# Kernel tuning notes

Measured on AMD Instinct MI355X. Metric: run time of the kernel, lower is better.

The kernel has to match this reference:

```python
import jax, jax.numpy as jnp
import numpy as np
import math

N = 20000          # nodes (residues)
E = 640000         # edges
CS = 384           # c_s
CZ = 128           # c_z
CH = 16            # c_hidden
H = 8              # no_heads
PQK = 8            # no_qk_points == no_v_points (forced equal, see notes)
FS = 128           # scalar channels in feat_irreps
PIN = 16           # vector channels in feat_irreps
HC = H * CH        # 128
HPQ = H * PQK * 3  # 192
CZ4 = CZ // 4      # 32
OUT_IN = HC + 3 * H + H + H * CZ4  # 416 actual concat width
INF = 100000.0
EPS = 1e-8


def setup_inputs() -> dict:
    key = jax.random.key(0)
    ks = jax.random.split(key, 16)
    w = lambda k, i, o: (jax.random.normal(k, (i, o), jnp.float32) / np.float32(np.sqrt(i)))
    frame_s = jax.random.normal(ks[0], (N, CS), jnp.float32)
    tfn_t = jax.random.normal(ks[1], (N, FS + 3 * PIN), jnp.float32)
    z = jax.random.normal(ks[2], (E, CZ), jnp.float32)
    edge_index = jax.random.randint(ks[3], (2, E), 0, N)
    mask = jnp.ones((N,), jnp.float32)
    # Rigid transforms: proper-ish rotations via QR, translations
    rot, _ = jnp.linalg.qr(jax.random.normal(ks[4], (N, 3, 3), jnp.float32))
    trans = jax.random.normal(ks[5], (N, 3), jnp.float32)
    return {
        "frame_s": frame_s, "tfn_t": tfn_t, "z": z,
        "edge_index": edge_index, "mask": mask,
        "rot": rot, "trans": trans,
        "Wq": w(ks[6], CS, HC), "bq": jnp.zeros((HC,), jnp.float32),
        "Wk_s": w(ks[7], FS, HC), "Wk_v": w(ks[8], PIN, PQK),
        "Wqp": w(ks[9], CS, HPQ), "bqp": jnp.zeros((HPQ,), jnp.float32),
        "Wb": w(ks[10], CZ, H), "bb": jnp.zeros((H,), jnp.float32),
        "Wdz": w(ks[11], CZ, CZ4), "bdz": jnp.zeros((CZ4,), jnp.float32),
        # ipa_point_weights_init_: softplus(hw) == 1  =>  hw = log(e - 1)
        "head_weights": jnp.full((H,), np.float32(np.log(np.e - 1.0))),
        "Wout": w(ks[12], OUT_IN, CS), "bout": jnp.zeros((CS,), jnp.float32),
    }


def _segment_softmax(a, seg, n):
    # pyg-style numerically stable segment softmax over edges grouped by seg
    m = jax.ops.segment_max(a, seg, num_segments=n)
    m = jnp.where(jnp.isfinite(m), m, 0.0)
    e = jnp.exp(a - m[seg])
    s = jax.ops.segment_sum(e, seg, num_segments=n)
    return e / (s[seg] + 1e-16)


def _forward(frame_s, tfn_t, z, mask, rot, trans,
             Wq, bq, Wk_s, Wk_v, Wqp, bqp, Wb, bb, Wdz, bdz,
             head_weights, Wout, bout, edge_index):
    n = frame_s.shape[0]
    src = edge_index[1]
    dst = edge_index[0]

    # scalar queries: [N,H,C]
    q = (frame_s @ Wq + bq).reshape(n, H, CH)

    # o3.Linear (feat_irreps -> k_irreps): scalars mix scalars, vectors mix vectors.
    # NOTE: original code uses linear_k for BOTH k and v (faithful bug), so v==k.
    scal = tfn_t[:, :FS]
    vecs = tfn_t[:, FS:].reshape(n, PIN, 3)
    k_scal = scal @ Wk_s                                   # [N, HC]
    k_vec = jnp.einsum('npx,pq->nqx', vecs, Wk_v)          # [N, PQK, 3]
    k = k_scal.reshape(n, H, CH)
    v = k
    k_tail = k_vec.reshape(n, PQK * 3)                     # [N, 24]
    # torch: split([3]*PQK) then stack(dim=-1) -> [N,3,PQK], then view [N,H,-1,3]
    k_pts = jnp.stack(jnp.split(k_tail, PQK, axis=-1), axis=-1)  # [N,3,PQK]
    k_pts = k_pts.reshape(n, H, -1, 3)                     # [N,H,1,3]
    v_pts = k_pts

    # query points, rigid-transformed: [N,H,PQK,3]
    q_pts = frame_s @ Wqp + bqp                            # [N, 3*H*PQK]
    q_pts = jnp.stack(jnp.split(q_pts, 3, axis=-1), axis=-1)  # [N, H*PQK, 3]
    q_pts = jnp.einsum('nij,npj->npi', rot, q_pts) + trans[:, None, :]
    q_pts = q_pts.reshape(n, H, PQK, 3)

    # scalar attention logits [E,H]
    a = jnp.einsum('ehc,ehc->eh', q[src], k[dst])
    a = a * np.float32(math.sqrt(1.0 / (3 * CH)))
    b = z @ Wb + bb                                        # [E,H]
    a = a + np.float32(math.sqrt(1.0 / 3)) * b

    # point attention: disp [E,H,PQK,3] (k_pts broadcasts over points)
    disp = q_pts[src] - k_pts[dst]
    pt_att = jnp.sum(disp * disp, axis=-1)                 # [E,H,PQK]
    hw = jax.nn.softplus(head_weights) * np.float32(math.sqrt(1.0 / (3 * (PQK * 9.0 / 2))))
    pt_att = -0.5 * jnp.sum(pt_att * hw[None, :, None], axis=-1)  # [E,H]

    edge_mask = INF * (mask[dst] * mask[src] - 1.0)        # [E]
    a = a + pt_att + edge_mask[:, None]

    a = _segment_softmax(a, src, n)                        # [E,H]

    # scalar output
    o = jax.ops.segment_sum(a[..., None] * v[dst], src, num_segments=n)  # [N,H,C]
    o = o.reshape(n, HC)

    # point output
    o_pt = jax.ops.segment_sum(a[:, :, None, None] * v_pts[dst], src, num_segments=n)  # [N,H,1,3]
    o_pt = jnp.einsum('nji,nhpj->nhpi', rot, o_pt - trans[:, None, None, :])  # invert_apply
    o_pt_norm = jnp.sqrt(jnp.sum(o_pt * o_pt, axis=-1) + EPS).reshape(n, H)
    o_pt = o_pt.reshape(n, -1, 3)                          # [N,H,3]

    # pair output
    pair_z = z @ Wdz + bdz                                 # [E,CZ4]
    o_pair = jax.ops.segment_sum(a[..., None] * pair_z[:, None, :], src, num_segments=n)  # [N,H,CZ4]
    o_pair = o_pair.reshape(n, H * CZ4)

    feats = jnp.concatenate(
        [o, o_pt[..., 0], o_pt[..., 1], o_pt[..., 2], o_pt_norm, o_pair], axis=-1)  # [N,416]
    return feats @ Wout + bout                             # [N, CS]


def reference(frame_s, tfn_t, z, edge_index, mask, rot, trans,
              Wq, bq, Wk_s, Wk_v, Wqp, bqp, Wb, bb, Wdz, bdz,
              head_weights, Wout, bout):
    return _forward(frame_s, tfn_t, z, mask, rot, trans,
                    Wq, bq, Wk_s, Wk_v, Wqp, bqp, Wb, bb, Wdz, bdz,
                    head_weights, Wout, bout, edge_index)
```

## Files before the change

kernel.cpp:

```cpp
#include <hip/hip_runtime.h>
#include <math.h>

typedef __attribute__((ext_vector_type(8))) short short8;
typedef __attribute__((ext_vector_type(4))) float f32x4;

static __device__ inline unsigned short f2bf(float f) {
    union { float f; unsigned u; } v; v.f = f;
    unsigned r = v.u + 0x7FFF + ((v.u >> 16) & 1);
    return (unsigned short)(r >> 16);
}

template<int WJ>
__device__ __forceinline__ void gemm_body(
    unsigned short* __restrict__ As, unsigned short* __restrict__ Bs,
    const float* __restrict__ A, int lda,
    const float* __restrict__ BT, int ldb,
    const float* __restrict__ bias,
    float* __restrict__ C, int ldc,
    int M, int N, int K, int bx, int by)
{
    constexpr int GBN = WJ * 32;
    const int t = threadIdx.x;
    const int wid = t >> 6, lane = t & 63;
    const int wm = (wid & 1) * 64;
    const int wn = (wid >> 1) * (WJ * 16);
    const int row16 = lane & 15, quad = lane >> 4;
    const int bm = bx * 128;
    const int bn = by * GBN;

    f32x4 acc[4][WJ];
    #pragma unroll
    for (int i = 0; i < 4; ++i)
        #pragma unroll
        for (int j = 0; j < WJ; ++j)
            #pragma unroll
            for (int r = 0; r < 4; ++r) acc[i][j][r] = 0.f;

    const int ktiles = (K + 63) >> 6;
    for (int kt = 0; kt < ktiles; ++kt) {
        const int k0 = kt << 6;
        #pragma unroll
        for (int it = 0; it < 8; ++it) {
            int f = it * 256 + t;
            int row = f >> 4, kq = (f & 15) << 2;
            float4 av = make_float4(0.f, 0.f, 0.f, 0.f);
            if (bm + row < M && k0 + kq < K)
                av = *(const float4*)(A + (size_t)(bm + row) * lda + k0 + kq);
            ushort4 uv;
            uv.x = f2bf(av.x); uv.y = f2bf(av.y); uv.z = f2bf(av.z); uv.w = f2bf(av.w);
            *(ushort4*)(&As[row * 72 + kq]) = uv;
        }
        #pragma unroll
        for (int it = 0; it < WJ * 2; ++it) {
            int f = it * 256 + t;
            int row = f >> 4, kq = (f & 15) << 2;
            float4 bv = make_float4(0.f, 0.f, 0.f, 0.f);
            if (bn + row < N && k0 + kq < K)
                bv = *(const float4*)(BT + (size_t)(bn + row) * ldb + k0 + kq);
            ushort4 uv;
            uv.x = f2bf(bv.x); uv.y = f2bf(bv.y); uv.z = f2bf(bv.z); uv.w = f2bf(bv.w);
            *(ushort4*)(&Bs[row * 72 + kq]) = uv;
        }
        __syncthreads();

        #pragma unroll
        for (int ks = 0; ks < 64; ks += 32) {
            short8 af[4], bfv[WJ];
            #pragma unroll
            for (int i = 0; i < 4; ++i)
                af[i] = *(const short8*)(&As[(wm + i * 16 + row16) * 72 + ks + quad * 8]);
            #pragma unroll
            for (int j = 0; j < WJ; ++j)
                bfv[j] = *(const short8*)(&Bs[(wn + j * 16 + row16) * 72 + ks + quad * 8]);
            #pragma unroll
            for (int i = 0; i < 4; ++i)
                #pragma unroll
                for (int j = 0; j < WJ; ++j)
                    acc[i][j] = __builtin_amdgcn_mfma_f32_16x16x32_bf16(af[i], bfv[j], acc[i][j], 0, 0, 0);
        }
        __syncthreads();
    }

    #pragma unroll
    for (int i = 0; i < 4; ++i)
        #pragma unroll
        for (int j = 0; j < WJ; ++j) {
            int col = bn + wn + j * 16 + row16;
            if (col >= N) continue;
            float bv = bias ? bias[col] : 0.f;
            #pragma unroll
            for (int r = 0; r < 4; ++r) {
                int row = bm + wm + i * 16 + quad * 4 + r;
                if (row < M) C[(size_t)row * ldc + col] = acc[i][j][r] + bv;
            }
        }
}

template<int WJ>
__global__ __launch_bounds__(256) void gemm_mfma(
    const float* __restrict__ A, int lda,
    const float* __restrict__ BT, int ldb,
    const float* __restrict__ bias,
    float* __restrict__ C, int ldc,
    int M, int N, int K)
{
    __shared__ unsigned short As[128 * 72];
    __shared__ unsigned short Bs[WJ * 32 * 72];
    gemm_body<WJ>(As, Bs, A, lda, BT, ldb, bias, C, ldc, M, N, K, blockIdx.x, blockIdx.y);
}

__global__ __launch_bounds__(256) void bpair_stream(
    const float* __restrict__ z, const float* __restrict__ wcatT,
    const float* __restrict__ bcat, float* __restrict__ bpair, int E)
{
    const int lane = threadIdx.x & 63;
    const int wid = threadIdx.x >> 6;
    const int row16 = lane & 15, quad = lane >> 4;

    short8 bfv[3][4];
    float bj[3];
    #pragma unroll
    for (int j = 0; j < 3; ++j) {
        int col = j * 16 + row16;
        bool cv = col < 40;
        bj[j] = cv ? bcat[col] : 0.f;
        #pragma unroll
        for (int ks = 0; ks < 4; ++ks) {
            float4 w0 = make_float4(0.f, 0.f, 0.f, 0.f);
            float4 w1 = make_float4(0.f, 0.f, 0.f, 0.f);
            if (cv) {
                const float* wp = wcatT + (size_t)col * 128 + ks * 32 + quad * 8;
                w0 = *(const float4*)(wp);
                w1 = *(const float4*)(wp + 4);
            }
            short8 f;
            f[0] = (short)f2bf(w0.x); f[1] = (short)f2bf(w0.y);
            f[2] = (short)f2bf(w0.z); f[3] = (short)f2bf(w0.w);
            f[4] = (short)f2bf(w1.x); f[5] = (short)f2bf(w1.y);
            f[6] = (short)f2bf(w1.z); f[7] = (short)f2bf(w1.w);
            bfv[j][ks] = f;
        }
    }

    const int nstrips = (E + 31) >> 5;
    const int gw = blockIdx.x * 4 + wid;
    const int nw = gridDim.x * 4;
    for (int st = gw; st < nstrips; st += nw) {
        const int r0 = st * 32;
        short8 af[2][4];
        #pragma unroll
        for (int i = 0; i < 2; ++i) {
            int row = r0 + i * 16 + row16;
            bool rv = row < E;
            const float* zp = z + (size_t)row * 128 + quad * 8;
            #pragma unroll
            for (int ks = 0; ks < 4; ++ks) {
                float4 a0 = make_float4(0.f, 0.f, 0.f, 0.f);
                float4 a1 = make_float4(0.f, 0.f, 0.f, 0.f);
                if (rv) {
                    a0 = *(const float4*)(zp + ks * 32);
                    a1 = *(const float4*)(zp + ks * 32 + 4);
                }
                short8 f;
                f[0] = (short)f2bf(a0.x); f[1] = (short)f2bf(a0.y);
                f[2] = (short)f2bf(a0.z); f[3] = (short)f2bf(a0.w);
                f[4] = (short)f2bf(a1.x); f[5] = (short)f2bf(a1.y);
                f[6] = (short)f2bf(a1.z); f[7] = (short)f2bf(a1.w);
                af[i][ks] = f;
            }
        }

        f32x4 acc[2][3];
        #pragma unroll
        for (int i = 0; i < 2; ++i)
            #pragma unroll
            for (int j = 0; j < 3; ++j)
                #pragma unroll
                for (int r = 0; r < 4; ++r) acc[i][j][r] = 0.f;

        #pragma unroll
        for (int ks = 0; ks < 4; ++ks)
            #pragma unroll
            for (int i = 0; i < 2; ++i)
                #pragma unroll
                for (int j = 0; j < 3; ++j)
                    acc[i][j] = __builtin_amdgcn_mfma_f32_16x16x32_bf16(af[i][ks], bfv[j][ks], acc[i][j], 0, 0, 0);

        #pragma unroll
        for (int i = 0; i < 2; ++i)
            #pragma unroll
            for (int j = 0; j < 3; ++j) {
                int col = j * 16 + row16;
                if (col >= 40) continue;
                #pragma unroll
                for (int r = 0; r < 4; ++r) {
                    int row = r0 + i * 16 + quad * 4 + r;
                    if (row < E) bpair[(size_t)row * 40 + col] = acc[i][j][r] + bj[j];
                }
            }
    }
}

__global__ __launch_bounds__(256) void mega_kernel(
    const float* __restrict__ frame_s, const float* __restrict__ wqqpT,
    const float* __restrict__ bqqp, float* __restrict__ qqp, int n,
    const float* __restrict__ tfn, const float* __restrict__ wksT,
    float* __restrict__ kbuf,
    const float* __restrict__ Wkv, float* __restrict__ kpts,
    const int* __restrict__ srcA, int* __restrict__ cur, int* __restrict__ elist, int E,
    int nb_qqp_x, int nb_qqp, int nb_k, int nb_kpts)
{
    __shared__ unsigned short As[128 * 72];
    __shared__ unsigned short Bs[128 * 72];
    int b = blockIdx.x;
    if (b < nb_qqp) {
        gemm_body<4>(As, Bs, frame_s, 384, wqqpT, 384, bqqp, qqp, 320, n, 320, 384,
                     b % nb_qqp_x, b / nb_qqp_x);
        return;
    }
    b -= nb_qqp;
    if (b < nb_k) {
        gemm_body<4>(As, Bs, tfn, 176, wksT, 128, nullptr, kbuf, 128, n, 128, 128, b, 0);
        return;
    }
    b -= nb_k;
    if (b < nb_kpts) {
        int t = b * 256 + threadIdx.x;
        if (t < n * 24) {
            int node = t / 24, f = t % 24;
            int a = f >> 3;
            int bb2 = f & 7;
            const float* vr = tfn + (size_t)node * 176 + 128;
            float s = 0.f;
            #pragma unroll
            for (int p = 0; p < 16; ++p) s += vr[p * 3 + a] * Wkv[p * 8 + bb2];
            kpts[t] = s;
        }
        return;
    }
    b -= nb_kpts;
    {
        int e = b * 256 + threadIdx.x;
        if (e < E) {
            int s = srcA[e];
            int pos = atomicAdd(&cur[s], 1);
            elist[pos] = e;
        }
    }
}

__global__ void prep_kernel(const float* __restrict__ Wq, const float* __restrict__ bq,
                            const float* __restrict__ Wqp, const float* __restrict__ bqp,
                            const float* __restrict__ Wb, const float* __restrict__ bb,
                            const float* __restrict__ Wdz, const float* __restrict__ bdz,
                            const float* __restrict__ Wks, const float* __restrict__ Wout,
                            float* __restrict__ wqqpT, float* __restrict__ bqqp,
                            float* __restrict__ wcatT, float* __restrict__ bcat,
                            float* __restrict__ wksT, float* __restrict__ woutT,
                            int* __restrict__ cnt, int n)
{
    const float SC_QK = 0.14433756729740643f;
    const float SC_B  = 0.5773502691896258f;
    int gid = blockIdx.x * 256 + threadIdx.x;
    int stride = gridDim.x * 256;
    for (int i = gid; i < n; i += stride) cnt[i] = 0;
    for (int i = gid; i < 320 * 384; i += stride) {
        int o = i / 384, c = i % 384;
        wqqpT[i] = (o < 128) ? Wq[c * 128 + o] * SC_QK : Wqp[c * 192 + (o - 128)];
    }
    for (int i = gid; i < 320; i += stride) bqqp[i] = (i < 128) ? bq[i] * SC_QK : bqp[i - 128];
    for (int i = gid; i < 40 * 128; i += stride) {
        int o = i >> 7, c = i & 127;
        wcatT[i] = (o < 8) ? Wb[c * 8 + o] * SC_B : Wdz[c * 32 + (o - 8)];
    }
    for (int i = gid; i < 40; i += stride) bcat[i] = (i < 8) ? bb[i] * SC_B : bdz[i - 8];
    for (int i = gid; i < 128 * 128; i += stride) {
        int o = i >> 7, c = i & 127;
        wksT[i] = Wks[c * 128 + o];
    }
    for (int i = gid; i < 384 * 416; i += stride) {
        int o = i / 416, c = i % 416;
        woutT[i] = Wout[c * 384 + o];
    }
}

__global__ void count_kernel(const int* __restrict__ srcA, int* __restrict__ cnt, int E)
{
    int e = blockIdx.x * 256 + threadIdx.x;
    if (e < E) atomicAdd(&cnt[srcA[e]], 1);
}

__global__ void scan_kernel(const int* __restrict__ cnt, int* __restrict__ off,
                            int* __restrict__ cur, int n)
{
    __shared__ int sums[1024];
    int t = threadIdx.x;
    int chunk = (n + 1023) >> 10;
    int begin = t * chunk;
    int local = 0;
    for (int j = 0; j < chunk; ++j) {
        int i = begin + j;
        if (i < n) local += cnt[i];
    }
    sums[t] = local;
    __syncthreads();
    for (int d = 1; d < 1024; d <<= 1) {
        int x = sums[t];
        int y = (t >= d) ? sums[t - d] : 0;
        __syncthreads();
        sums[t] = x + y;
        __syncthreads();
    }
    int run = sums[t] - local;
    for (int j = 0; j < chunk; ++j) {
        int i = begin + j;
        if (i < n) {
            off[i] = run;
            cur[i] = run;
            run += cnt[i];
        }
    }
}

__global__ __launch_bounds__(256) void attn_kernel(
    const int* __restrict__ off, const int* __restrict__ cnt,
    const int* __restrict__ elist, const int* __restrict__ dstA,
    const float* __restrict__ qqp, const float* __restrict__ kbuf,
    const float* __restrict__ kpts,
    const float* __restrict__ bpair, const float* __restrict__ mask,
    const float* __restrict__ hwin,
    const float* __restrict__ rot, const float* __restrict__ trans,
    float* __restrict__ feats, int n)
{
    int wave = threadIdx.x >> 6;
    int lane = threadIdx.x & 63;
    int s = blockIdx.x * 4 + wave;
    if (s >= n) return;
    int es = lane >> 3;
    int h  = lane & 7;

    float qh[16];
    {
        const float* qp = qqp + (size_t)s * 320 + h * 16;
        #pragma unroll
        for (int c = 0; c < 16; ++c) qh[c] = qp[c];
    }
    const float* Rp = rot + (size_t)s * 9;
    const float* Tp = trans + (size_t)s * 3;
    float R0 = Rp[0], R1 = Rp[1], R2 = Rp[2];
    float R3 = Rp[3], R4 = Rp[4], R5 = Rp[5];
    float R6 = Rp[6], R7 = Rp[7], R8 = Rp[8];
    float T0 = Tp[0], T1 = Tp[1], T2 = Tp[2];
    float qpt[24];
    {
        const float* qr = qqp + (size_t)s * 320 + 128 + h * 8;
        #pragma unroll
        for (int p2 = 0; p2 < 8; ++p2) {
            float c0 = qr[p2], c1 = qr[64 + p2], c2 = qr[128 + p2];
            qpt[p2 * 3 + 0] = R0 * c0 + R1 * c1 + R2 * c2 + T0;
            qpt[p2 * 3 + 1] = R3 * c0 + R4 * c1 + R5 * c2 + T1;
            qpt[p2 * 3 + 2] = R6 * c0 + R7 * c1 + R8 * c2 + T2;
        }
    }
    float hwv = log1pf(__expf(hwin[h])) * 0.04811252243246882f;
    float mask_s = mask[s];
    int myoff = off[s], mycnt = cnt[s];

    float ssum = 0.f;
    float oacc[16];
    #pragma unroll
    for (int c = 0; c < 16; ++c) oacc[c] = 0.f;
    float optacc[3] = {0.f, 0.f, 0.f};
    float opacc[8][4];
    #pragma unroll
    for (int j = 0; j < 8; ++j)
        #pragma unroll
        for (int c = 0; c < 4; ++c) opacc[j][c] = 0.f;

    int nb = (mycnt + 7) >> 3;
    for (int b = 0; b < nb; ++b) {
        int idx = b * 8 + es;
        bool valid = idx < mycnt;
        int e = valid ? elist[myoff + idx] : 0;
        int d = dstA[e];

        const float* kr = kbuf + (size_t)d * 128 + h * 16;
        float4 ka = *(const float4*)(kr + 0);
        float4 kb = *(const float4*)(kr + 4);
        float4 kc = *(const float4*)(kr + 8);
        float4 kd = *(const float4*)(kr + 12);

        const float* kp = kpts + (size_t)d * 24 + h * 3;
        float kp0 = kp[0], kp1 = kp[1], kp2 = kp[2];

        const float* bp = bpair + (size_t)e * 40;
        float bh = bp[h];
        float4 pair4 = *(const float4*)(bp + 8 + h * 4);

        float qk = qh[0] * ka.x + qh[1] * ka.y + qh[2] * ka.z + qh[3] * ka.w
                 + qh[4] * kb.x + qh[5] * kb.y + qh[6] * kb.z + qh[7] * kb.w
                 + qh[8] * kc.x + qh[9] * kc.y + qh[10] * kc.z + qh[11] * kc.w
                 + qh[12] * kd.x + qh[13] * kd.y + qh[14] * kd.z + qh[15] * kd.w;

        float pt = 0.f;
        #pragma unroll
        for (int pp = 0; pp < 8; ++pp) {
            float d0 = qpt[pp * 3 + 0] - kp0;
            float d1 = qpt[pp * 3 + 1] - kp1;
            float d2 = qpt[pp * 3 + 2] - kp2;
            pt += d0 * d0 + d1 * d1 + d2 * d2;
        }

        float md = mask[d];
        float logit = qk + bh - hwv * pt + 100000.0f * (mask_s * md - 1.0f);
        float w = valid ? __expf(logit) : 0.f;

        ssum += w;
        oacc[0] += w * ka.x; oacc[1] += w * ka.y; oacc[2] += w * ka.z; oacc[3] += w * ka.w;
        oacc[4] += w * kb.x; oacc[5] += w * kb.y; oacc[6] += w * kb.z; oacc[7] += w * kb.w;
        oacc[8] += w * kc.x; oacc[9] += w * kc.y; oacc[10] += w * kc.z; oacc[11] += w * kc.w;
        oacc[12] += w * kd.x; oacc[13] += w * kd.y; oacc[14] += w * kd.z; oacc[15] += w * kd.w;
        optacc[0] += w * kp0;
        optacc[1] += w * kp1;
        optacc[2] += w * kp2;

        #pragma unroll
        for (int jh = 0; jh < 8; ++jh) {
            float wj = __shfl(w, (es << 3) + jh);
            opacc[jh][0] += wj * pair4.x;
            opacc[jh][1] += wj * pair4.y;
            opacc[jh][2] += wj * pair4.z;
            opacc[jh][3] += wj * pair4.w;
        }
    }

    #pragma unroll
    for (int delta = 8; delta <= 32; delta <<= 1) {
        ssum += __shfl_xor(ssum, delta);
        #pragma unroll
        for (int c = 0; c < 16; ++c) oacc[c] += __shfl_xor(oacc[c], delta);
        #pragma unroll
        for (int i = 0; i < 3; ++i) optacc[i] += __shfl_xor(optacc[i], delta);
        #pragma unroll
        for (int j = 0; j < 8; ++j)
            #pragma unroll
            for (int c = 0; c < 4; ++c) opacc[j][c] += __shfl_xor(opacc[j][c], delta);
    }

    float invj[8];
    #pragma unroll
    for (int jh = 0; jh < 8; ++jh)
        invj[jh] = 1.f / (__shfl(ssum, jh) + 1e-16f);

    if (es == 0) {
        float inv = 1.f / (ssum + 1e-16f);
        float* f = feats + (size_t)s * 416;
        #pragma unroll
        for (int c = 0; c < 16; c += 4) {
            float4 v = make_float4(oacc[c] * inv, oacc[c + 1] * inv, oacc[c + 2] * inv, oacc[c + 3] * inv);
            *(float4*)(&f[h * 16 + c]) = v;
        }
        float v0 = optacc[0] * inv - T0;
        float v1 = optacc[1] * inv - T1;
        float v2 = optacc[2] * inv - T2;
        float r0 = R0 * v0 + R3 * v1 + R6 * v2;
        float r1 = R1 * v0 + R4 * v1 + R7 * v2;
        float r2 = R2 * v0 + R5 * v1 + R8 * v2;
        f[128 + h] = r0;
        f[136 + h] = r1;
        f[144 + h] = r2;
        f[152 + h] = sqrtf(r0 * r0 + r1 * r1 + r2 * r2 + 1e-8f);
        #pragma unroll
        for (int jh = 0; jh < 8; ++jh) {
            float4 v = make_float4(opacc[jh][0] * invj[jh], opacc[jh][1] * invj[jh],
                                   opacc[jh][2] * invj[jh], opacc[jh][3] * invj[jh]);
            *(float4*)(&f[160 + jh * 32 + h * 4]) = v;
        }
    }
}

extern "C" void kernel_launch(void* const* d_in, const int* in_sizes, int n_in,
                              void* d_out, int out_size, void* d_ws, size_t ws_size,
                              hipStream_t stream)
{
    const float* frame_s = (const float*)d_in[0];
    const float* tfn     = (const float*)d_in[1];
    const float* z       = (const float*)d_in[2];
    const int*   ei      = (const int*)d_in[3];
    const float* mask    = (const float*)d_in[4];
    const float* rot     = (const float*)d_in[5];
    const float* trans   = (const float*)d_in[6];
    const float* Wq      = (const float*)d_in[7];
    const float* bq      = (const float*)d_in[8];
    const float* Wks     = (const float*)d_in[9];
    const float* Wkv     = (const float*)d_in[10];
    const float* Wqp     = (const float*)d_in[11];
    const float* bqp     = (const float*)d_in[12];
    const float* Wb      = (const float*)d_in[13];
    const float* bb      = (const float*)d_in[14];
    const float* Wdz     = (const float*)d_in[15];
    const float* bdz     = (const float*)d_in[16];
    const float* hw      = (const float*)d_in[17];
    const float* Wout    = (const float*)d_in[18];
    const float* bout    = (const float*)d_in[19];
    float* out = (float*)d_out;

    int n = in_sizes[0] / 384;
    int E = in_sizes[3] / 2;
    const int* dstA = ei;
    const int* srcA = ei + E;

    float* ws = (float*)d_ws;
    size_t p = 0;
    auto alloc = [&](size_t elems) -> float* {
        float* r = ws + p;
        p += (elems + 15) & ~((size_t)15);
        return r;
    };
    float* qqpbuf = alloc((size_t)n * 320);
    float* kbuf   = alloc((size_t)n * 128);
    float* kpts   = alloc((size_t)n * 24);
    float* feats  = alloc((size_t)n * 416);
    float* bpair  = alloc((size_t)E * 40);
    float* wqqpT  = alloc(320 * 384);
    float* bqqp   = alloc(320);
    float* wcatT  = alloc(40 * 128);
    float* bcat   = alloc(64);
    float* wksT   = alloc(128 * 128);
    float* woutT  = alloc(384 * 416);
    int* cnt   = (int*)alloc((size_t)n);
    int* off   = (int*)alloc((size_t)n);
    int* cur   = (int*)alloc((size_t)n);
    int* elist = (int*)alloc((size_t)E);

    prep_kernel<<<512, 256, 0, stream>>>(Wq, bq, Wqp, bqp, Wb, bb, Wdz, bdz, Wks, Wout,
                                         wqqpT, bqqp, wcatT, bcat, wksT, woutT, cnt, n);

    count_kernel<<<(E + 255) / 256, 256, 0, stream>>>(srcA, cnt, E);
    scan_kernel<<<1, 1024, 0, stream>>>(cnt, off, cur, n);

    bpair_stream<<<2048, 256, 0, stream>>>(z, wcatT, bcat, bpair, E);

    int nb_qqp_x = (n + 127) / 128;
    int nb_qqp   = nb_qqp_x * 3;
    int nb_k     = (n + 127) / 128;
    int nb_kpts  = (n * 24 + 255) / 256;
    int nb_fill  = (E + 255) / 256;
    int nb_total = nb_qqp + nb_k + nb_kpts + nb_fill;
    mega_kernel<<<nb_total, 256, 0, stream>>>(
        frame_s, wqqpT, bqqp, qqpbuf, n,
        tfn, wksT, kbuf,
        Wkv, kpts,
        srcA, cur, elist, E,
        nb_qqp_x, nb_qqp, nb_k, nb_kpts);

    attn_kernel<<<(n + 3) / 4, 256, 0, stream>>>(off, cnt, elist, dstA,
                                                 qqpbuf, kbuf, kpts, bpair, mask, hw,
                                                 rot, trans, feats, n);

    {
        dim3 g((n + 127) / 128, 3);
        gemm_mfma<4><<<g, 256, 0, stream>>>(feats, 416, woutT, 416, bout, out, 384, n, 384, 416);
    }
    (void)n_in; (void)out_size; (void)ws_size;
}
```

Measured before the change: 856.9 us.

## Fuse bpair into mega kernel, merge count into prep, pack edge info

Folds the bpair edge GEMM into the mega_kernel block-dispatch, merges the count kernel into the weight prep kernel, and replaces the cnt zeroing with a memset. The edge list now stores (edge, dst) pairs, so attention no longer does a dependent dstA gather, and it prefetches the next edge pair one iteration ahead. The aim is fewer kernel launches, more overlap between independent stages, and a shorter dependent-load chain in the attention loop. In exchange the mega kernel carries more register and LDS pressure from the bpair path, and the edge list takes twice the memory.

```diff
diff --git a/kernel.cpp b/kernel.cpp
--- a/kernel.cpp
+++ b/kernel.cpp
@@ -109,9 +109,10 @@
     gemm_body<WJ>(As, Bs, A, lda, BT, ldb, bias, C, ldc, M, N, K, blockIdx.x, blockIdx.y);
 }
 
-__global__ __launch_bounds__(256) void bpair_stream(
+__device__ __forceinline__ void bpair_body(
     const float* __restrict__ z, const float* __restrict__ wcatT,
-    const float* __restrict__ bcat, float* __restrict__ bpair, int E)
+    const float* __restrict__ bcat, float* __restrict__ bpair, int E,
+    int bb, int nbb)
 {
     const int lane = threadIdx.x & 63;
     const int wid = threadIdx.x >> 6;
@@ -143,8 +144,8 @@
     }
 
     const int nstrips = (E + 31) >> 5;
-    const int gw = blockIdx.x * 4 + wid;
-    const int nw = gridDim.x * 4;
+    const int gw = bb * 4 + wid;
+    const int nw = nbb * 4;
     for (int st = gw; st < nstrips; st += nw) {
         const int r0 = st * 32;
         short8 af[2][4];
@@ -202,17 +203,25 @@
 }
 
 __global__ __launch_bounds__(256) void mega_kernel(
+    const float* __restrict__ z, const float* __restrict__ wcatT,
+    const float* __restrict__ bcat, float* __restrict__ bpair, int E,
     const float* __restrict__ frame_s, const float* __restrict__ wqqpT,
     const float* __restrict__ bqqp, float* __restrict__ qqp, int n,
     const float* __restrict__ tfn, const float* __restrict__ wksT,
     float* __restrict__ kbuf,
     const float* __restrict__ Wkv, float* __restrict__ kpts,
-    const int* __restrict__ srcA, int* __restrict__ cur, int* __restrict__ elist, int E,
-    int nb_qqp_x, int nb_qqp, int nb_k, int nb_kpts)
+    const int* __restrict__ srcA, const int* __restrict__ dstA,
+    int* __restrict__ cur, int2* __restrict__ einfo,
+    int nb_bp, int nb_qqp_x, int nb_qqp, int nb_k, int nb_kpts)
 {
     __shared__ unsigned short As[128 * 72];
     __shared__ unsigned short Bs[128 * 72];
     int b = blockIdx.x;
+    if (b < nb_bp) {
+        bpair_body(z, wcatT, bcat, bpair, E, b, nb_bp);
+        return;
+    }
+    b -= nb_bp;
     if (b < nb_qqp) {
         gemm_body<4>(As, Bs, frame_s, 384, wqqpT, 384, bqqp, qqp, 320, n, 320, 384,
                      b % nb_qqp_x, b / nb_qqp_x);
@@ -244,26 +253,33 @@
         if (e < E) {
             int s = srcA[e];
             int pos = atomicAdd(&cur[s], 1);
-            elist[pos] = e;
-        }
-    }
-}
-
-__global__ void prep_kernel(const float* __restrict__ Wq, const float* __restrict__ bq,
-                            const float* __restrict__ Wqp, const float* __restrict__ bqp,
-                            const float* __restrict__ Wb, const float* __restrict__ bb,
-                            const float* __restrict__ Wdz, const float* __restrict__ bdz,
-                            const float* __restrict__ Wks, const float* __restrict__ Wout,
-                            float* __restrict__ wqqpT, float* __restrict__ bqqp,
-                            float* __restrict__ wcatT, float* __restrict__ bcat,
-                            float* __restrict__ wksT, float* __restrict__ woutT,
-                            int* __restrict__ cnt, int n)
-{
+            einfo[pos] = make_int2(e, dstA[e]);
+        }
+    }
+}
+
+__global__ void prep_count_kernel(
+    const float* __restrict__ Wq, const float* __restrict__ bq,
+    const float* __restrict__ Wqp, const float* __restrict__ bqp,
+    const float* __restrict__ Wb, const float* __restrict__ bb,
+    const float* __restrict__ Wdz, const float* __restrict__ bdz,
+    const float* __restrict__ Wks, const float* __restrict__ Wout,
+    float* __restrict__ wqqpT, float* __restrict__ bqqp,
+    float* __restrict__ wcatT, float* __restrict__ bcat,
+    float* __restrict__ wksT, float* __restrict__ woutT,
+    const int* __restrict__ srcA, int* __restrict__ cnt, int E, int nb_cnt)
+{
+    int b = blockIdx.x;
+    if (b < nb_cnt) {
+        int e = b * 256 + threadIdx.x;
+        if (e < E) atomicAdd(&cnt[srcA[e]], 1);
+        return;
+    }
+    b -= nb_cnt;
     const float SC_QK = 0.14433756729740643f;
     const float SC_B  = 0.5773502691896258f;
-    int gid = blockIdx.x * 256 + threadIdx.x;
-    int stride = gridDim.x * 256;
-    for (int i = gid; i < n; i += stride) cnt[i] = 0;
+    int gid = b * 256 + threadIdx.x;
+    int stride = (gridDim.x - nb_cnt) * 256;
     for (int i = gid; i < 320 * 384; i += stride) {
         int o = i / 384, c = i % 384;
         wqqpT[i] = (o < 128) ? Wq[c * 128 + o] * SC_QK : Wqp[c * 192 + (o - 128)];
@@ -282,12 +298,6 @@
         int o = i / 416, c = i % 416;
         woutT[i] = Wout[c * 384 + o];
     }
-}
-
-__global__ void count_kernel(const int* __restrict__ srcA, int* __restrict__ cnt, int E)
-{
-    int e = blockIdx.x * 256 + threadIdx.x;
-    if (e < E) atomicAdd(&cnt[srcA[e]], 1);
 }
 
 __global__ void scan_kernel(const int* __restrict__ cnt, int* __restrict__ off,
@@ -324,7 +334,7 @@
 
 __global__ __launch_bounds__(256) void attn_kernel(
     const int* __restrict__ off, const int* __restrict__ cnt,
-    const int* __restrict__ elist, const int* __restrict__ dstA,
+    const int2* __restrict__ einfo,
     const float* __restrict__ qqp, const float* __restrict__ kbuf,
     const float* __restrict__ kpts,
     const float* __restrict__ bpair, const float* __restrict__ mask,
@@ -378,11 +388,21 @@
         for (int c = 0; c < 4; ++c) opacc[j][c] = 0.f;
 
     int nb = (mycnt + 7) >> 3;
+    int2 ed = make_int2(0, 0);
+    if (nb > 0) {
+        int pos0 = (es < mycnt) ? myoff + es : (mycnt > 0 ? myoff : 0);
+        ed = einfo[pos0];
+    }
     for (int b = 0; b < nb; ++b) {
         int idx = b * 8 + es;
         bool valid = idx < mycnt;
-        int e = valid ? elist[myoff + idx] : 0;
-        int d = dstA[e];
+        int e = ed.x, d = ed.y;
+        int2 ned = ed;
+        if (b + 1 < nb) {
+            int nidx = idx + 8;
+            int npos = (nidx < mycnt) ? myoff + nidx : myoff;
+            ned = einfo[npos];
+        }
 
         const float* kr = kbuf + (size_t)d * 128 + h * 16;
         float4 ka = *(const float4*)(kr + 0);
@@ -432,6 +452,7 @@
             opacc[jh][2] += wj * pair4.z;
             opacc[jh][3] += wj * pair4.w;
         }
+        ed = ned;
     }
 
     #pragma unroll
@@ -528,33 +549,37 @@
     float* bcat   = alloc(64);
     float* wksT   = alloc(128 * 128);
     float* woutT  = alloc(384 * 416);
-    int* cnt   = (int*)alloc((size_t)n);
-    int* off   = (int*)alloc((size_t)n);
-    int* cur   = (int*)alloc((size_t)n);
-    int* elist = (int*)alloc((size_t)E);
-
-    prep_kernel<<<512, 256, 0, stream>>>(Wq, bq, Wqp, bqp, Wb, bb, Wdz, bdz, Wks, Wout,
-                                         wqqpT, bqqp, wcatT, bcat, wksT, woutT, cnt, n);
-
-    count_kernel<<<(E + 255) / 256, 256, 0, stream>>>(srcA, cnt, E);
+    int*  cnt   = (int*)alloc((size_t)n);
+    int*  off   = (int*)alloc((size_t)n);
+    int*  cur   = (int*)alloc((size_t)n);
+    int2* einfo = (int2*)alloc((size_t)E * 2);
+
+    hipMemsetAsync(cnt, 0, (size_t)n * sizeof(int), stream);
+
+    int nb_cnt = (E + 255) / 256;
+    prep_count_kernel<<<nb_cnt + 512, 256, 0, stream>>>(
+        Wq, bq, Wqp, bqp, Wb, bb, Wdz, bdz, Wks, Wout,
+        wqqpT, bqqp, wcatT, bcat, wksT, woutT,
+        srcA, cnt, E, nb_cnt);
+
     scan_kernel<<<1, 1024, 0, stream>>>(cnt, off, cur, n);
 
-    bpair_stream<<<2048, 256, 0, stream>>>(z, wcatT, bcat, bpair, E);
-
+    int nb_bp    = 2048;
     int nb_qqp_x = (n + 127) / 128;
     int nb_qqp   = nb_qqp_x * 3;
     int nb_k     = (n + 127) / 128;
     int nb_kpts  = (n * 24 + 255) / 256;
     int nb_fill  = (E + 255) / 256;
-    int nb_total = nb_qqp + nb_k + nb_kpts + nb_fill;
+    int nb_total = nb_bp + nb_qqp + nb_k + nb_kpts + nb_fill;
     mega_kernel<<<nb_total, 256, 0, stream>>>(
+        z, wcatT, bcat, bpair, E,
         frame_s, wqqpT, bqqp, qqpbuf, n,
         tfn, wksT, kbuf,
         Wkv, kpts,
-        srcA, cur, elist, E,
-        nb_qqp_x, nb_qqp, nb_k, nb_kpts);
-
-    attn_kernel<<<(n + 3) / 4, 256, 0, stream>>>(off, cnt, elist, dstA,
+        srcA, dstA, cur, einfo,
+        nb_bp, nb_qqp_x, nb_qqp, nb_k, nb_kpts);
+
+    attn_kernel<<<(n + 3) / 4, 256, 0, stream>>>(off, cnt, einfo,
                                                  qqpbuf, kbuf, kpts, bpair, mask, hw,
                                                  rot, trans, feats, n);
 
```

After: 815.6 us. 1.05x faster.
